# Kernel tuning notes

Hardware: AMD Instinct MI355X
Metric: run time of the kernel (lower is better)

Reference implementation:

```python
import jax, jax.numpy as jnp
import numpy as np

T, B, IN, H, OUT = 128, 1024, 47, 646, 5

def setup_inputs() -> dict:
    key = jax.random.key(0)
    ks = jax.random.split(key, 11)
    s_in = 1.0 / np.sqrt(H)
    return {
        "xs": jax.random.normal(ks[0], (T, B, IN), dtype=jnp.float32),
        "W_ih0": jax.random.normal(ks[1], (H, IN), dtype=jnp.float32) * s_in,
        "W_hh0": jax.random.normal(ks[2], (H, H), dtype=jnp.float32) * s_in,
        "b_ih0": jax.random.normal(ks[3], (H,), dtype=jnp.float32) * s_in,
        "b_hh0": jax.random.normal(ks[4], (H,), dtype=jnp.float32) * s_in,
        "W_ih1": jax.random.normal(ks[5], (H, H), dtype=jnp.float32) * s_in,
        "W_hh1": jax.random.normal(ks[6], (H, H), dtype=jnp.float32) * s_in,
        "b_ih1": jax.random.normal(ks[7], (H,), dtype=jnp.float32) * s_in,
        "b_hh1": jax.random.normal(ks[8], (H,), dtype=jnp.float32) * s_in,
        "W_out": jax.random.normal(ks[9], (OUT, H), dtype=jnp.float32) * s_in,
        "b_out": jnp.zeros((OUT,), dtype=jnp.float32),
    }

def reference(xs, W_ih0, W_hh0, b_ih0, b_hh0, W_ih1, W_hh1, b_ih1, b_hh1, W_out, b_out):
    batch = xs.shape[1]
    h0 = jnp.zeros((batch, H), dtype=xs.dtype)
    h1 = jnp.zeros((batch, H), dtype=xs.dtype)

    def step(carry, x_t):
        h0, h1 = carry
        # layer 0: Elman cell, tanh
        h0 = jnp.tanh(x_t @ W_ih0.T + b_ih0 + h0 @ W_hh0.T + b_hh0)
        # layer 1 consumes layer 0's output at this timestep
        h1 = jnp.tanh(h0 @ W_ih1.T + b_ih1 + h1 @ W_hh1.T + b_hh1)
        return (h0, h1), None

    (h0, h1), _ = jax.lax.scan(step, (h0, h1), xs)
    # classifier on last layer's final hidden state
    logits = h1 @ W_out.T + b_out  # [B, 5]
    return logits
```

## Files before the change

### kernel.cpp

```cpp
#include <hip/hip_runtime.h>
#include <hip/hip_bf16.h>

#define T_STEPS 128
#define B_SZ    1024
#define IN_SZ   47
#define H_SZ    646
#define OUT_SZ  5

#define XK    96
#define K0    768
#define K1    1344
#define N0PAD 704
#define N1PAD 672
#define RING  17
#define SLAB  172032
#define FSTR  160

#define NL0B  7
#define NL1B  14
#define NBLK  (8 * (NL0B + NL1B))

typedef __hip_bfloat16 bf16;
typedef unsigned short ush;
using frag8 = __attribute__((ext_vector_type(8))) short;
using f32x4 = __attribute__((ext_vector_type(4))) float;


__global__ void prep_xs(const float* __restrict__ xs, bf16* __restrict__ xs_pad) {
    int idx = blockIdx.x * blockDim.x + threadIdx.x;
    if (idx >= T_STEPS * B_SZ * XK) return;
    int k = idx % XK;
    int rb = idx / XK;
    float v = (k < IN_SZ) ? xs[(size_t)rb * IN_SZ + k] : 0.f;
    xs_pad[idx] = __float2bfloat16(v);
}

__global__ void pack_w0(const float* __restrict__ Wih, const float* __restrict__ Whh,
                        bf16* __restrict__ Wc) {
    int idx = blockIdx.x * blockDim.x + threadIdx.x;
    if (idx >= N0PAD * K0) return;
    int j = idx / K0, k = idx % K0;
    float v = 0.f;
    if (j < H_SZ) {
        if (k < IN_SZ)                      v = Wih[(size_t)j * IN_SZ + k];
        else if (k >= XK && k < XK + H_SZ)  v = Whh[(size_t)j * H_SZ + (k - XK)];
    }
    Wc[idx] = __float2bfloat16(v);
}

__global__ void pack_w1(const float* __restrict__ Wih, const float* __restrict__ Whh,
                        bf16* __restrict__ Wc) {
    int idx = blockIdx.x * blockDim.x + threadIdx.x;
    if (idx >= N1PAD * K1) return;
    int j = idx / K1, k = idx % K1;
    float v = 0.f;
    if (j < H_SZ) {
        if (k < H_SZ)                          v = Wih[(size_t)j * H_SZ + k];
        else if (k >= 672 && k < 672 + H_SZ)   v = Whh[(size_t)j * H_SZ + (k - 672)];
    }
    Wc[idx] = __float2bfloat16(v);
}

__global__ void pack_bias(const float* __restrict__ bi, const float* __restrict__ bh,
                          float* __restrict__ b, int n) {
    int j = blockIdx.x * blockDim.x + threadIdx.x;
    if (j >= n) return;
    b[j] = (j < H_SZ) ? (bi[j] + bh[j]) : 0.f;
}


__device__ __forceinline__ void tanh_store(ush* dst, float x) {
    x = fminf(fmaxf(x, -15.f), 15.f);
    float e = __expf(2.f * x);
    bf16 hb = __float2bfloat16((e - 1.f) / (e + 1.f));
    *dst = *(ush*)&hb;
}

__device__ __forceinline__ void poll_ge(int* p, int need) {
    while (__hip_atomic_load(p, __ATOMIC_RELAXED, __HIP_MEMORY_SCOPE_AGENT) < need)
        __builtin_amdgcn_s_sleep(2);
}

__global__ __launch_bounds__(512, 2) void persist(
    const bf16* __restrict__ xs_pad, const bf16* __restrict__ Wc0,
    const bf16* __restrict__ Wc1, const float* __restrict__ b0,
    const float* __restrict__ b1, bf16* __restrict__ Sring,
    int* __restrict__ flags)
{
    extern __shared__ ush Wlds[];
    const int bid  = blockIdx.x;
    const int rg   = bid & 7;
    const int c8   = bid >> 3;
    const bool isL0 = (c8 < NL0B);
    const int tid  = threadIdx.x;
    const int wv   = tid >> 6;
    const int lane = tid & 63;
    const int q8   = (lane >> 4) * 8;
    const int l15  = lane & 15;

    if (isL0) {
        const int col0 = c8 * 96;
        for (int g = wv; g < 144; g += 8) {
            int kc = g / 6, ct = g % 6;
            const bf16* src = Wc0 + (size_t)(col0 + ct*16 + l15) * K0 + kc*32 + q8;
            *(uint4*)&Wlds[g*512 + lane*8] = *(const uint4*)src;
        }
    } else {
        const int col0 = (c8 - NL0B) * 48;
        for (int g = wv; g < 126; g += 8) {
            int kc = g / 3, ct = g % 3;
            const bf16* src = Wc1 + (size_t)(col0 + ct*16 + l15) * K1 + kc*32 + q8;
            *(uint4*)&Wlds[g*512 + lane*8] = *(const uint4*)src;
        }
    }
    __syncthreads();

    const int loc = wv * 16 + l15;
    bf16* const ringbase = Sring + (size_t)rg * RING * SLAB;
    int*  const fL0 = flags + rg * FSTR;
    int*  const fL1 = flags + (8 + rg) * FSTR;

    if (isL0) {
        const int col0 = c8 * 96;
        float bias[6];
        #pragma unroll
        for (int ct = 0; ct < 6; ++ct) bias[ct] = b0[col0 + ct*16 + l15];

        for (int p = 0; p < 128; ++p) {
            const bf16* rsl = ringbase + (size_t)((p + RING - 1) % RING) * SLAB;
            bf16*       wsl = ringbase + (size_t)(p % RING) * SLAB;

            const bf16* xr = xs_pad + ((size_t)p * B_SZ + rg*128 + loc) * XK + q8;
            uint4 xbuf[3];
            #pragma unroll
            for (int i = 0; i < 3; ++i) xbuf[i] = *(const uint4*)(xr + i*32);

            if (tid == 0) {
                if (p > 0)   poll_ge(&fL0[p-1], NL0B);
                if (p >= 17) poll_ge(&fL1[p-16], NL1B);
            }
            __syncthreads();
            if (p >= RING + 1 && (p - 1) % RING == 0)
                __builtin_amdgcn_fence(__ATOMIC_ACQUIRE, "agent");

            const bf16* hr = rsl + (size_t)loc * K1 + q8;
            uint4 hbuf[21];
            #pragma unroll
            for (int i = 0; i < 21; ++i) hbuf[i] = *(const uint4*)(hr + i*32);

            f32x4 acc[6] = {};
            #pragma unroll
            for (int kc = 0; kc < 24; ++kc) {
                frag8 af = (kc < 3) ? *(const frag8*)&xbuf[kc]
                                    : *(const frag8*)&hbuf[kc-3];
                #pragma unroll
                for (int ct = 0; ct < 6; ++ct) {
                    frag8 wf = *(const frag8*)&Wlds[(kc*6+ct)*512 + lane*8];
                    acc[ct] = __builtin_amdgcn_mfma_f32_16x16x32_bf16(
                        af, wf, acc[ct], 0, 0, 0);
                }
            }
            const int rbase = wv*16 + (lane>>4)*4;
            #pragma unroll
            for (int ct = 0; ct < 6; ++ct) {
                const int col = col0 + ct*16 + l15;
                if (col < H_SZ) {
                    #pragma unroll
                    for (int i = 0; i < 4; ++i)
                        tanh_store((ush*)(wsl + (size_t)(rbase+i)*K1 + col),
                                   acc[ct][i] + bias[ct]);
                }
            }
            __syncthreads();
            if (tid == 0)
                __hip_atomic_fetch_add(&fL0[p], 1, __ATOMIC_RELAXED,
                                       __HIP_MEMORY_SCOPE_AGENT);
        }
    } else {
        const int col0 = (c8 - NL0B) * 48;
        float bias[3];
        #pragma unroll
        for (int ct = 0; ct < 3; ++ct) bias[ct] = b1[col0 + ct*16 + l15];

        for (int q = 1; q <= 128; ++q) {
            const bf16* rsl = ringbase + (size_t)((q + RING - 1) % RING) * SLAB;
            bf16*       wsl = ringbase + (size_t)(q % RING) * SLAB;
            const bf16* ar  = rsl + (size_t)loc * K1 + q8;

            if (tid == 0) poll_ge(&fL0[q-1], NL0B);
            __syncthreads();
            if (q >= RING + 1 && (q - 1) % RING == 0)
                __builtin_amdgcn_fence(__ATOMIC_ACQUIRE, "agent");

            uint4 h0buf[21];
            #pragma unroll
            for (int i = 0; i < 21; ++i) h0buf[i] = *(const uint4*)(ar + i*32);
            f32x4 acc[3] = {};
            #pragma unroll
            for (int kc = 0; kc < 21; ++kc) {
                frag8 af = *(const frag8*)&h0buf[kc];
                #pragma unroll
                for (int ct = 0; ct < 3; ++ct) {
                    frag8 wf = *(const frag8*)&Wlds[(kc*3+ct)*512 + lane*8];
                    acc[ct] = __builtin_amdgcn_mfma_f32_16x16x32_bf16(
                        af, wf, acc[ct], 0, 0, 0);
                }
            }

            if (q > 1) {
                if (tid == 0) poll_ge(&fL1[q-1], NL1B);
                __syncthreads();
            }
            uint4 h1buf[21];
            #pragma unroll
            for (int i = 0; i < 21; ++i)
                h1buf[i] = *(const uint4*)(ar + (21 + i)*32);
            #pragma unroll
            for (int kc = 21; kc < 42; ++kc) {
                frag8 af = *(const frag8*)&h1buf[kc-21];
                #pragma unroll
                for (int ct = 0; ct < 3; ++ct) {
                    frag8 wf = *(const frag8*)&Wlds[(kc*3+ct)*512 + lane*8];
                    acc[ct] = __builtin_amdgcn_mfma_f32_16x16x32_bf16(
                        af, wf, acc[ct], 0, 0, 0);
                }
            }
            const int rbase = wv*16 + (lane>>4)*4;
            #pragma unroll
            for (int ct = 0; ct < 3; ++ct) {
                const int col = col0 + ct*16 + l15;
                if (col < H_SZ) {
                    #pragma unroll
                    for (int i = 0; i < 4; ++i)
                        tanh_store((ush*)(wsl + (size_t)(rbase+i)*K1 + 672 + col),
                                   acc[ct][i] + bias[ct]);
                }
            }
            __syncthreads();
            if (tid == 0)
                __hip_atomic_fetch_add(&fL1[q], 1, __ATOMIC_RELAXED,
                                       __HIP_MEMORY_SCOPE_AGENT);
        }
    }
}

__global__ __launch_bounds__(256) void classifier(
    const bf16* __restrict__ Sring, const float* __restrict__ Wout,
    const float* __restrict__ bout, float* __restrict__ out)
{
    const int wave = threadIdx.x >> 6, lane = threadIdx.x & 63;
    const int row = blockIdx.x * 4 + wave;
    const int rg = row >> 7, loc = row & 127;
    const bf16* h1 = Sring + ((size_t)rg * RING + (128 % RING)) * SLAB
                     + (size_t)loc * K1 + 672;
    float acc[OUT_SZ] = {0.f, 0.f, 0.f, 0.f, 0.f};
    for (int k = lane; k < H_SZ; k += 64) {
        float h = __bfloat162float(h1[k]);
        #pragma unroll
        for (int o = 0; o < OUT_SZ; ++o) acc[o] += h * Wout[(size_t)o * H_SZ + k];
    }
    #pragma unroll
    for (int o = 0; o < OUT_SZ; ++o) {
        float v = acc[o];
        #pragma unroll
        for (int off = 32; off; off >>= 1) v += __shfl_down(v, off, 64);
        if (lane == 0) out[(size_t)row * OUT_SZ + o] = v + bout[o];
    }
}


extern "C" void kernel_launch(void* const* d_in, const int* in_sizes, int n_in,
                              void* d_out, int out_size, void* d_ws, size_t ws_size,
                              hipStream_t stream) {
    const float* xs   = (const float*)d_in[0];
    const float* Wih0 = (const float*)d_in[1];
    const float* Whh0 = (const float*)d_in[2];
    const float* bih0 = (const float*)d_in[3];
    const float* bhh0 = (const float*)d_in[4];
    const float* Wih1 = (const float*)d_in[5];
    const float* Whh1 = (const float*)d_in[6];
    const float* bih1 = (const float*)d_in[7];
    const float* bhh1 = (const float*)d_in[8];
    const float* Wout = (const float*)d_in[9];
    const float* bout = (const float*)d_in[10];
    float* out = (float*)d_out;

    char* ws = (char*)d_ws;
    size_t off = 0;
    bf16* xs_pad = (bf16*)(ws + off); off += (size_t)T_STEPS * B_SZ * XK * 2;
    bf16* Wc0    = (bf16*)(ws + off); off += (size_t)N0PAD * K0 * 2;
    bf16* Wc1    = (bf16*)(ws + off); off += (size_t)N1PAD * K1 * 2;
    float* b0    = (float*)(ws + off); off += (size_t)N0PAD * 4;
    float* b1    = (float*)(ws + off); off += (size_t)N1PAD * 4;
    bf16* Sring  = (bf16*)(ws + off); off += (size_t)8 * RING * SLAB * 2;
    int*  flags  = (int*)(ws + off);  off += (size_t)16 * FSTR * 4;

    hipMemsetAsync(Sring, 0, (size_t)8 * RING * SLAB * 2, stream);
    hipMemsetAsync(flags, 0, (size_t)16 * FSTR * 4, stream);

    prep_xs <<<(T_STEPS * B_SZ * XK + 255) / 256, 256, 0, stream>>>(xs, xs_pad);
    pack_w0 <<<(N0PAD * K0 + 255) / 256, 256, 0, stream>>>(Wih0, Whh0, Wc0);
    pack_w1 <<<(N1PAD * K1 + 255) / 256, 256, 0, stream>>>(Wih1, Whh1, Wc1);
    pack_bias<<<(N0PAD + 255) / 256, 256, 0, stream>>>(bih0, bhh0, b0, N0PAD);
    pack_bias<<<(N1PAD + 255) / 256, 256, 0, stream>>>(bih1, bhh1, b1, N1PAD);

    hipFuncSetAttribute((const void*)persist,
                        hipFuncAttributeMaxDynamicSharedMemorySize, 147456);
    void* args[] = { (void*)&xs_pad, (void*)&Wc0, (void*)&Wc1, (void*)&b0,
                     (void*)&b1, (void*)&Sring, (void*)&flags };
    hipLaunchCooperativeKernel((const void*)persist, dim3(NBLK), dim3(512),
                               args, 147456, stream);

    classifier<<<B_SZ / 4, 256, 0, stream>>>(Sring, Wout, bout, out);
}
```

Measured before the change: 1.620 ms.

## Split row groups to half-blocks with per-wave flag polling instead of block barriers

Each 512-thread block now serves two independent 64-row groups, one per half of its waves, with 16 row groups and their own ring buffers and flags. Each wave polls the producer counters itself and publishes with a waitcnt plus a per-wave atomic increment, which removes the block-wide __syncthreads around every step. The goal is finer-grained dependency tracking so waves do not stall on the slowest wave in the block. The cost is more atomic traffic and polling per step, and correctness now depends on per-wave release ordering through a relaxed atomic after waitcnt.

```diff
diff --git a/kernel.cpp b/kernel.cpp
--- a/kernel.cpp
+++ b/kernel.cpp
@@ -13,12 +13,16 @@
 #define N0PAD 704
 #define N1PAD 672
 #define RING  17
-#define SLAB  172032
+#define NRG   16
+#define SLAB2 86016
 #define FSTR  160
 
 #define NL0B  7
 #define NL1B  14
 #define NBLK  (8 * (NL0B + NL1B))
+
+#define PUB0  (NL0B * 4)
+#define PUB1  (NL1B * 4)
 
 typedef __hip_bfloat16 bf16;
 typedef unsigned short ush;
@@ -89,7 +93,7 @@
 {
     extern __shared__ ush Wlds[];
     const int bid  = blockIdx.x;
-    const int rg   = bid & 7;
+    const int rgp  = bid & 7;
     const int c8   = bid >> 3;
     const bool isL0 = (c8 < NL0B);
     const int tid  = threadIdx.x;
@@ -115,10 +119,11 @@
     }
     __syncthreads();
 
-    const int loc = wv * 16 + l15;
-    bf16* const ringbase = Sring + (size_t)rg * RING * SLAB;
+    const int rg  = rgp * 2 + (wv >> 2);
+    const int loc = (wv & 3) * 16 + l15;
+    bf16* const ringbase = Sring + (size_t)rg * RING * SLAB2;
     int*  const fL0 = flags + rg * FSTR;
-    int*  const fL1 = flags + (8 + rg) * FSTR;
+    int*  const fL1 = flags + (NRG + rg) * FSTR;
 
     if (isL0) {
         const int col0 = c8 * 96;
@@ -127,19 +132,18 @@
         for (int ct = 0; ct < 6; ++ct) bias[ct] = b0[col0 + ct*16 + l15];
 
         for (int p = 0; p < 128; ++p) {
-            const bf16* rsl = ringbase + (size_t)((p + RING - 1) % RING) * SLAB;
-            bf16*       wsl = ringbase + (size_t)(p % RING) * SLAB;
-
-            const bf16* xr = xs_pad + ((size_t)p * B_SZ + rg*128 + loc) * XK + q8;
+            const bf16* rsl = ringbase + (size_t)((p + RING - 1) % RING) * SLAB2;
+            bf16*       wsl = ringbase + (size_t)(p % RING) * SLAB2;
+
+            const bf16* xr = xs_pad + ((size_t)p * B_SZ + rg*64 + loc) * XK + q8;
             uint4 xbuf[3];
             #pragma unroll
             for (int i = 0; i < 3; ++i) xbuf[i] = *(const uint4*)(xr + i*32);
 
-            if (tid == 0) {
-                if (p > 0)   poll_ge(&fL0[p-1], NL0B);
-                if (p >= 17) poll_ge(&fL1[p-16], NL1B);
-            }
-            __syncthreads();
+            if (lane == 0) {
+                if (p > 0)   poll_ge(&fL0[p-1], PUB0);
+                if (p >= 17) poll_ge(&fL1[p-16], PUB1);
+            }
             if (p >= RING + 1 && (p - 1) % RING == 0)
                 __builtin_amdgcn_fence(__ATOMIC_ACQUIRE, "agent");
 
@@ -160,7 +164,7 @@
                         af, wf, acc[ct], 0, 0, 0);
                 }
             }
-            const int rbase = wv*16 + (lane>>4)*4;
+            const int rbase = (wv & 3)*16 + (lane>>4)*4;
             #pragma unroll
             for (int ct = 0; ct < 6; ++ct) {
                 const int col = col0 + ct*16 + l15;
@@ -171,8 +175,8 @@
                                    acc[ct][i] + bias[ct]);
                 }
             }
-            __syncthreads();
-            if (tid == 0)
+            __builtin_amdgcn_s_waitcnt(0);
+            if (lane == 0)
                 __hip_atomic_fetch_add(&fL0[p], 1, __ATOMIC_RELAXED,
                                        __HIP_MEMORY_SCOPE_AGENT);
         }
@@ -183,12 +187,11 @@
         for (int ct = 0; ct < 3; ++ct) bias[ct] = b1[col0 + ct*16 + l15];
 
         for (int q = 1; q <= 128; ++q) {
-            const bf16* rsl = ringbase + (size_t)((q + RING - 1) % RING) * SLAB;
-            bf16*       wsl = ringbase + (size_t)(q % RING) * SLAB;
+            const bf16* rsl = ringbase + (size_t)((q + RING - 1) % RING) * SLAB2;
+            bf16*       wsl = ringbase + (size_t)(q % RING) * SLAB2;
             const bf16* ar  = rsl + (size_t)loc * K1 + q8;
 
-            if (tid == 0) poll_ge(&fL0[q-1], NL0B);
-            __syncthreads();
+            if (lane == 0) poll_ge(&fL0[q-1], PUB0);
             if (q >= RING + 1 && (q - 1) % RING == 0)
                 __builtin_amdgcn_fence(__ATOMIC_ACQUIRE, "agent");
 
@@ -207,10 +210,7 @@
                 }
             }
 
-            if (q > 1) {
-                if (tid == 0) poll_ge(&fL1[q-1], NL1B);
-                __syncthreads();
-            }
+            if (q > 1) { if (lane == 0) poll_ge(&fL1[q-1], PUB1); }
             uint4 h1buf[21];
             #pragma unroll
             for (int i = 0; i < 21; ++i)
@@ -225,7 +225,7 @@
                         af, wf, acc[ct], 0, 0, 0);
                 }
             }
-            const int rbase = wv*16 + (lane>>4)*4;
+            const int rbase = (wv & 3)*16 + (lane>>4)*4;
             #pragma unroll
             for (int ct = 0; ct < 3; ++ct) {
                 const int col = col0 + ct*16 + l15;
@@ -236,8 +236,8 @@
                                    acc[ct][i] + bias[ct]);
                 }
             }
-            __syncthreads();
-            if (tid == 0)
+            __builtin_amdgcn_s_waitcnt(0);
+            if (lane == 0)
                 __hip_atomic_fetch_add(&fL1[q], 1, __ATOMIC_RELAXED,
                                        __HIP_MEMORY_SCOPE_AGENT);
         }
@@ -250,8 +250,8 @@
 {
     const int wave = threadIdx.x >> 6, lane = threadIdx.x & 63;
     const int row = blockIdx.x * 4 + wave;
-    const int rg = row >> 7, loc = row & 127;
-    const bf16* h1 = Sring + ((size_t)rg * RING + (128 % RING)) * SLAB
+    const int rg = row >> 6, loc = row & 63;
+    const bf16* h1 = Sring + ((size_t)rg * RING + (128 % RING)) * SLAB2
                      + (size_t)loc * K1 + 672;
     float acc[OUT_SZ] = {0.f, 0.f, 0.f, 0.f, 0.f};
     for (int k = lane; k < H_SZ; k += 64) {
@@ -292,11 +292,11 @@
     bf16* Wc1    = (bf16*)(ws + off); off += (size_t)N1PAD * K1 * 2;
     float* b0    = (float*)(ws + off); off += (size_t)N0PAD * 4;
     float* b1    = (float*)(ws + off); off += (size_t)N1PAD * 4;
-    bf16* Sring  = (bf16*)(ws + off); off += (size_t)8 * RING * SLAB * 2;
-    int*  flags  = (int*)(ws + off);  off += (size_t)16 * FSTR * 4;
-
-    hipMemsetAsync(Sring, 0, (size_t)8 * RING * SLAB * 2, stream);
-    hipMemsetAsync(flags, 0, (size_t)16 * FSTR * 4, stream);
+    bf16* Sring  = (bf16*)(ws + off); off += (size_t)NRG * RING * SLAB2 * 2;
+    int*  flags  = (int*)(ws + off);  off += (size_t)2 * NRG * FSTR * 4;
+
+    hipMemsetAsync(Sring, 0, (size_t)NRG * RING * SLAB2 * 2, stream);
+    hipMemsetAsync(flags, 0, (size_t)2 * NRG * FSTR * 4, stream);
 
     prep_xs <<<(T_STEPS * B_SZ * XK + 255) / 256, 256, 0, stream>>>(xs, xs_pad);
     pack_w0 <<<(N0PAD * K0 + 255) / 256, 256, 0, stream>>>(Wih0, Whh0, Wc0);
```

Measured after the change: 1.791 ms. 1.11x slower.
